# Optimization experiments

Hardware: AMD Instinct MI355X
Metric: run time of the kernel (lower is better)

Reference implementation:

```python
import jax, jax.numpy as jnp
import numpy as np

N_NODES = 100000
N_EDGES = 1600000
D_FEAT = 64


def setup_inputs() -> dict:
    key = jax.random.key(0)
    k1, k2, k3, k4, k5 = jax.random.split(key, 5)
    feat = jax.random.normal(k1, (N_NODES, D_FEAT), dtype=jnp.float32)
    weight = jax.random.normal(k2, (N_EDGES, 1), dtype=jnp.float32)
    bias = jax.random.normal(k3, (D_FEAT,), dtype=jnp.float32)
    src = jax.random.randint(k4, (N_EDGES,), 0, N_NODES, dtype=jnp.int32)
    dst = jax.random.randint(k5, (N_EDGES,), 0, N_NODES, dtype=jnp.int32)
    return {"feat": feat, "weight": weight, "bias": bias, "src": src, "dst": dst}


def reference(feat, weight, bias, src, dst):
    # Weighted SpMM: out[v] = sum_{e: dst[e]==v} weight[e] * feat[src[e]] + bias
    messages = feat[src] * weight  # [E, D] gather + per-edge scale
    out = jax.ops.segment_sum(messages, dst, num_segments=N_NODES)  # [N, D]
    return out + bias
```

## Files before the change

### kernel.cpp

```cpp
#include <hip/hip_runtime.h>

#define N_NODES 100000
#define N_EDGES 1600000
#define D_FEAT  64
#define NFEAT_ELEM (N_NODES * D_FEAT)

#define BUCK_SHIFT 6
#define BUCK_NODES 64
#define NBUCK ((N_NODES + BUCK_NODES - 1) / BUCK_NODES)
#define NB1 (NBUCK + 1)

#define CHUNK   8192
#define NCHUNK  ((N_EDGES + CHUNK - 1) / CHUNK)
#define BIN_BLK 512
#define BIN_EPT (CHUNK / BIN_BLK)
#define SCAN_PER ((NBUCK + BIN_BLK - 1) / BIN_BLK)
#define PREP_BLOCKS 128

#define GB_BLK   512
#define GB_NODES 128
#define NGRP ((NBUCK + 1) / 2)
#define GB_CAP   2816
#define GB_EPT   6

typedef float          vf4 __attribute__((ext_vector_type(4)));
typedef float          vf2 __attribute__((ext_vector_type(2)));
typedef int            vi2 __attribute__((ext_vector_type(2)));
typedef unsigned short vu4 __attribute__((ext_vector_type(4)));
typedef unsigned short ushort_t;

#define TBL_BYTES  (NCHUNK * NB1 * 2)
#define OFF_TBL    0
#define OFF_EP     (((OFF_TBL + TBL_BYTES) + 255) & ~255)
#define OFF_FEATB  (OFF_EP + N_EDGES * 8)
#define WS_MED     (size_t)OFF_FEATB
#define WS_FULL    (size_t)(OFF_FEATB + (size_t)NFEAT_ELEM * 2)

template <int BF16>
__global__ __launch_bounds__(BIN_BLK) void k_bin(const int* __restrict__ src,
                                                 const int* __restrict__ dst,
                                                 const float* __restrict__ weight,
                                                 const float* __restrict__ feat,
                                                 ushort_t* __restrict__ featb,
                                                 ushort_t* __restrict__ tbl,
                                                 vi2* __restrict__ ep) {
    if (blockIdx.x >= NCHUNK) {
        if (!BF16) return;
        const int stride = PREP_BLOCKS * BIN_BLK;
        for (int i = (blockIdx.x - NCHUNK) * BIN_BLK + threadIdx.x;
             i < NFEAT_ELEM / 4; i += stride) {
            vf4 x = ((const vf4*)feat)[i];
            vu4 r;
#pragma unroll
            for (int k = 0; k < 4; ++k) {
                unsigned bb = __float_as_uint(x[k]);
                r[k] = (ushort_t)((bb + 0x7fffu + ((bb >> 16) & 1u)) >> 16);
            }
            ((vu4*)featb)[i] = r;
        }
        return;
    }

    __shared__ vi2 schunk[CHUNK];
    __shared__ int lcnt[NBUCK];
    __shared__ int ss[BIN_BLK];
    const int t = threadIdx.x;
    const int c = blockIdx.x;
    const int e0 = c * CHUNK;
    const int chunkN = (N_EDGES - e0 < CHUNK) ? (N_EDGES - e0) : CHUNK;

    for (int i = t; i < NBUCK; i += BIN_BLK) lcnt[i] = 0;
    __syncthreads();

    int bk[BIN_EPT], rk[BIN_EPT], xk[BIN_EPT], wk[BIN_EPT];
#pragma unroll
    for (int k = 0; k < BIN_EPT; ++k) {
        const int e = e0 + t + k * BIN_BLK;
        bk[k] = -1;
        if (e < N_EDGES) {
            int v = __builtin_nontemporal_load(dst + e);
            int s = __builtin_nontemporal_load(src + e);
            wk[k] = __builtin_nontemporal_load((const int*)weight + e);
            bk[k] = v >> BUCK_SHIFT;
            xk[k] = ((v & (BUCK_NODES - 1)) << 24) | s;
            rk[k] = atomicAdd(&lcnt[bk[k]], 1);
        }
    }
    __syncthreads();

    int v7[SCAN_PER];
    const int lo = t * SCAN_PER;
    int s = 0;
#pragma unroll
    for (int k = 0; k < SCAN_PER; ++k) {
        const int i = lo + k;
        v7[k] = (i < NBUCK) ? lcnt[i] : 0;
        s += v7[k];
    }
    ss[t] = s;
    __syncthreads();
    for (int off = 1; off < BIN_BLK; off <<= 1) {
        int x = (t >= off) ? ss[t - off] : 0;
        __syncthreads();
        ss[t] += x;
        __syncthreads();
    }
    int run = ss[t] - s;
    ushort_t* row = tbl + (size_t)c * NB1;
#pragma unroll
    for (int k = 0; k < SCAN_PER; ++k) {
        const int i = lo + k;
        if (i < NBUCK) {
            row[i] = (ushort_t)run;
            lcnt[i] = run;
            run += v7[k];
        }
    }
    if (t == BIN_BLK - 1) row[NBUCK] = (ushort_t)chunkN;
    __syncthreads();

#pragma unroll
    for (int k = 0; k < BIN_EPT; ++k)
        if (bk[k] >= 0) schunk[lcnt[bk[k]] + rk[k]] = (vi2){xk[k], wk[k]};
    __syncthreads();

    for (int i = t; i < chunkN; i += BIN_BLK)
        ep[e0 + i] = schunk[i];
}

template <int BF16>
__global__ __launch_bounds__(GB_BLK, 8) void k_sgather(const float* __restrict__ feat,
                                                       const ushort_t* __restrict__ featb,
                                                       const float* __restrict__ bias,
                                                       const ushort_t* __restrict__ tbl,
                                                       const vi2* __restrict__ ep,
                                                       float* __restrict__ out) {
    __shared__ vi2      srt[GB_CAP];
    __shared__ int      basearr[GB_BLK];
    __shared__ ushort_t o0arr[GB_BLK];
    __shared__ ushort_t o1arr[GB_BLK];
    __shared__ int      cnt[GB_NODES], off[GB_NODES];
    __shared__ int      wsum[8];
    __shared__ int      wpre[9];
    __shared__ int      c64tot;

    const int t = threadIdx.x;
    const int lane = t & 63;
    const int wid = t >> 6;
    const int grp = blockIdx.x;
    const int b0 = grp * 2;
    if (t < GB_NODES) cnt[t] = 0;

    int o0 = 0, o1 = 0, o2 = 0;
    if (t < NCHUNK) {
        const ushort_t* rowp = tbl + (size_t)t * NB1 + b0;
        unsigned u = *(const unsigned*)rowp;
        o0 = (int)(u & 0xFFFFu);
        o1 = (int)(u >> 16);
        o2 = (b0 + 2 <= NBUCK) ? (int)rowp[2] : o1;
    }
    o0arr[t] = (ushort_t)o0;
    o1arr[t] = (ushort_t)o1;
    const int len = o2 - o0;

    int incl = len;
#pragma unroll
    for (int o = 1; o < 64; o <<= 1) {
        int x = __shfl_up(incl, o);
        if (lane >= o) incl += x;
    }
    if (lane == 63) wsum[wid] = incl;
    __syncthreads();
    if (t == 0) {
        int run = 0;
#pragma unroll
        for (int i2 = 0; i2 < 8; ++i2) { wpre[i2] = run; run += wsum[i2]; }
        wpre[8] = run;
    }
    __syncthreads();
    const int nTot = wpre[8];
    basearr[t] = wpre[wid] + incl - len;
    __syncthreads();

    const int nStg = nTot < GB_CAP ? nTot : GB_CAP;
    int   xk[GB_EPT];
    float wk[GB_EPT];
    int   rk[GB_EPT];
#pragma unroll
    for (int k = 0; k < GB_EPT; ++k) {
        const int p = t + k * GB_BLK;
        xk[k] = -1;
        if (p < nStg) {
            int c = 0;
#pragma unroll
            for (int s2 = 256; s2 > 0; s2 >>= 1) {
                int m = c + s2;
                if (m < GB_BLK && basearr[m] <= p) c = m;
            }
            const int e = (int)o0arr[c] + (p - basearr[c]);
            vi2 v = ep[(size_t)c * CHUNK + e];
            int r = ((e >= (int)o1arr[c]) ? 64 : 0) + (int)((unsigned)v.x >> 24);
            xk[k] = (v.x & 0xFFFFFF) | (r << 24);
            wk[k] = __int_as_float(v.y);
            rk[k] = atomicAdd(&cnt[r], 1);
        }
    }
    __syncthreads();

    {
        int v = (t < GB_NODES) ? cnt[t] : 0;
        int inc2 = v;
#pragma unroll
        for (int o = 1; o < 64; o <<= 1) {
            int x = __shfl_up(inc2, o);
            if (lane >= o) inc2 += x;
        }
        if (t == 63) c64tot = inc2;
        __syncthreads();
        if (t >= 64 && t < 128) inc2 += c64tot;
        if (t < GB_NODES) off[t] = inc2;
        __syncthreads();
    }

#pragma unroll
    for (int k = 0; k < GB_EPT; ++k) {
        if (xk[k] != -1) {
            int r = (unsigned)xk[k] >> 24;
            srt[off[r] - cnt[r] + rk[k]] = (vi2){xk[k], __float_as_int(wk[k])};
        }
    }
    __syncthreads();

    const int col = lane & 31;
    const int half = lane >> 5;
    const vf2 b2 = ((const vf2*)bias)[col];
    for (int rp = 0; rp < 8; ++rp) {
        const int rA = wid * 16 + rp;
        const int rB = rA + 8;
        const int ccA = cnt[rA], s0A = off[rA] - ccA;
        const int ccB = cnt[rB], s0B = off[rB] - ccB;
        float a0A = 0.f, a1A = 0.f, a0B = 0.f, a1B = 0.f;
        const int ccM = ccA > ccB ? ccA : ccB;
        for (int i = 0; i < ccM; i += 8) {
            float wA[4], wB[4];
            unsigned dA[4], dB[4];
            vf2 fA[4], fB[4];
#pragma unroll
            for (int k = 0; k < 4; ++k) {
                const int ei = i + 2 * k + half;
                vi2 e = (ei < ccA) ? srt[s0A + ei] : (vi2){0, 0};
                wA[k] = __int_as_float(e.y);
                const int sidx = e.x & 0xFFFFFF;
                if (BF16) dA[k] = *((const unsigned*)(featb + (size_t)sidx * D_FEAT) + col);
                else      fA[k] = *((const vf2*)(feat + (size_t)sidx * D_FEAT) + col);
            }
#pragma unroll
            for (int k = 0; k < 4; ++k) {
                const int ei = i + 2 * k + half;
                vi2 e = (ei < ccB) ? srt[s0B + ei] : (vi2){0, 0};
                wB[k] = __int_as_float(e.y);
                const int sidx = e.x & 0xFFFFFF;
                if (BF16) dB[k] = *((const unsigned*)(featb + (size_t)sidx * D_FEAT) + col);
                else      fB[k] = *((const vf2*)(feat + (size_t)sidx * D_FEAT) + col);
            }
            if (BF16) {
#pragma unroll
                for (int k = 0; k < 4; ++k) {
                    a0A = fmaf(wA[k], __uint_as_float(dA[k] << 16), a0A);
                    a1A = fmaf(wA[k], __uint_as_float(dA[k] & 0xFFFF0000u), a1A);
                    a0B = fmaf(wB[k], __uint_as_float(dB[k] << 16), a0B);
                    a1B = fmaf(wB[k], __uint_as_float(dB[k] & 0xFFFF0000u), a1B);
                }
            } else {
#pragma unroll
                for (int k = 0; k < 4; ++k) {
                    a0A = fmaf(wA[k], fA[k].x, a0A);
                    a1A = fmaf(wA[k], fA[k].y, a1A);
                    a0B = fmaf(wB[k], fB[k].x, a0B);
                    a1B = fmaf(wB[k], fB[k].y, a1B);
                }
            }
        }
        a0A += __shfl_xor(a0A, 32);
        a1A += __shfl_xor(a1A, 32);
        a0B += __shfl_xor(a0B, 32);
        a1B += __shfl_xor(a1B, 32);
        const int nodeA = grp * GB_NODES + rA;
        const int nodeB = grp * GB_NODES + rB;
        if (half == 0 && nodeA < N_NODES) {
            vf2 o = {a0A + b2.x, a1A + b2.y};
            __builtin_nontemporal_store(o, (vf2*)(out + (size_t)nodeA * D_FEAT) + col);
        }
        if (half == 0 && nodeB < N_NODES) {
            vf2 o = {a0B + b2.x, a1B + b2.y};
            __builtin_nontemporal_store(o, (vf2*)(out + (size_t)nodeB * D_FEAT) + col);
        }
    }
    __syncthreads();

    for (int p = GB_CAP + t; p < nTot; p += GB_BLK) {
        int c = 0;
#pragma unroll
        for (int s2 = 256; s2 > 0; s2 >>= 1) {
            int m = c + s2;
            if (m < GB_BLK && basearr[m] <= p) c = m;
        }
        const int e = (int)o0arr[c] + (p - basearr[c]);
        vi2 v = ep[(size_t)c * CHUNK + e];
        int r = ((e >= (int)o1arr[c]) ? 64 : 0) + (int)((unsigned)v.x >> 24);
        int node = grp * GB_NODES + r;
        float w = __int_as_float(v.y);
        int sidx = v.x & 0xFFFFFF;
        if (node < N_NODES)
            for (int d2 = 0; d2 < D_FEAT; ++d2)
                atomicAdd(&out[(size_t)node * D_FEAT + d2], w * feat[(size_t)sidx * D_FEAT + d2]);
    }
}

__global__ void init_out_kernel(const float* __restrict__ bias,
                                float* __restrict__ out) {
    int i = blockIdx.x * blockDim.x + threadIdx.x;
    if (i < N_NODES * D_FEAT) out[i] = bias[i & (D_FEAT - 1)];
}

__global__ void edge_scatter_kernel(const float* __restrict__ feat,
                                    const float* __restrict__ weight,
                                    const int* __restrict__ src,
                                    const int* __restrict__ dst,
                                    float* __restrict__ out) {
    int e = blockIdx.x * 4 + (threadIdx.x >> 6);
    int lane = threadIdx.x & 63;
    if (e < N_EDGES) {
        atomicAdd(&out[dst[e] * D_FEAT + lane], weight[e] * feat[src[e] * D_FEAT + lane]);
    }
}

extern "C" void kernel_launch(void* const* d_in, const int* in_sizes, int n_in,
                              void* d_out, int out_size, void* d_ws, size_t ws_size,
                              hipStream_t stream) {
    const float* feat   = (const float*)d_in[0];
    const float* weight = (const float*)d_in[1];
    const float* bias   = (const float*)d_in[2];
    const int*   src    = (const int*)d_in[3];
    const int*   dst    = (const int*)d_in[4];
    float* out = (float*)d_out;

    if (ws_size < WS_MED) {
        int total = N_NODES * D_FEAT;
        init_out_kernel<<<(total + 255) / 256, 256, 0, stream>>>(bias, out);
        edge_scatter_kernel<<<(N_EDGES + 3) / 4, 256, 0, stream>>>(feat, weight, src, dst, out);
        return;
    }

    char* ws = (char*)d_ws;
    ushort_t* tbl   = (ushort_t*)(ws + OFF_TBL);
    vi2*      ep    = (vi2*)(ws + OFF_EP);
    ushort_t* featb = (ushort_t*)(ws + OFF_FEATB);
    const bool use_bf16 = (ws_size >= WS_FULL);

    if (use_bf16) {
        k_bin<1><<<NCHUNK + PREP_BLOCKS, BIN_BLK, 0, stream>>>(src, dst, weight, feat, featb, tbl, ep);
        k_sgather<1><<<NGRP, GB_BLK, 0, stream>>>(feat, featb, bias, tbl, ep, out);
    } else {
        k_bin<0><<<NCHUNK, BIN_BLK, 0, stream>>>(src, dst, weight, feat, featb, tbl, ep);
        k_sgather<0><<<NGRP, GB_BLK, 0, stream>>>(feat, featb, bias, tbl, ep, out);
    }
}
```

Measured before the change: 64.08 us.

## Quantize gathered features to int8 with per-row scale folded into edge weight

Replaces the bf16 copy of the node features with an int8 copy that has one scale per row. The scale is multiplied into each edge weight during staging, so the gather loop reads 2 bytes per lane instead of 4 and converts int8 to float. This halves the random-gather traffic, at the cost of an extra scale lookup per edge and a large loss of precision that may break accuracy tolerance.

```diff
diff --git a/kernel.cpp b/kernel.cpp
--- a/kernel.cpp
+++ b/kernel.cpp
@@ -26,37 +26,46 @@
 typedef float          vf4 __attribute__((ext_vector_type(4)));
 typedef float          vf2 __attribute__((ext_vector_type(2)));
 typedef int            vi2 __attribute__((ext_vector_type(2)));
-typedef unsigned short vu4 __attribute__((ext_vector_type(4)));
 typedef unsigned short ushort_t;
+typedef signed char    s8_t;
 
 #define TBL_BYTES  (NCHUNK * NB1 * 2)
 #define OFF_TBL    0
 #define OFF_EP     (((OFF_TBL + TBL_BYTES) + 255) & ~255)
-#define OFF_FEATB  (OFF_EP + N_EDGES * 8)
-#define WS_MED     (size_t)OFF_FEATB
-#define WS_FULL    (size_t)(OFF_FEATB + (size_t)NFEAT_ELEM * 2)
-
-template <int BF16>
+#define OFF_SCALE  (OFF_EP + N_EDGES * 8)
+#define OFF_FEATQ  (OFF_SCALE + N_NODES * 4)
+#define WS_MED     (size_t)OFF_SCALE
+#define WS_FULL    (size_t)(OFF_FEATQ + (size_t)NFEAT_ELEM)
+
+template <int QNT>
 __global__ __launch_bounds__(BIN_BLK) void k_bin(const int* __restrict__ src,
                                                  const int* __restrict__ dst,
                                                  const float* __restrict__ weight,
                                                  const float* __restrict__ feat,
-                                                 ushort_t* __restrict__ featb,
+                                                 s8_t* __restrict__ featq,
+                                                 float* __restrict__ fscale,
                                                  ushort_t* __restrict__ tbl,
                                                  vi2* __restrict__ ep) {
+    const int t = threadIdx.x;
     if (blockIdx.x >= NCHUNK) {
-        if (!BF16) return;
-        const int stride = PREP_BLOCKS * BIN_BLK;
-        for (int i = (blockIdx.x - NCHUNK) * BIN_BLK + threadIdx.x;
-             i < NFEAT_ELEM / 4; i += stride) {
-            vf4 x = ((const vf4*)feat)[i];
-            vu4 r;
-#pragma unroll
-            for (int k = 0; k < 4; ++k) {
-                unsigned bb = __float_as_uint(x[k]);
-                r[k] = (ushort_t)((bb + 0x7fffu + ((bb >> 16) & 1u)) >> 16);
-            }
-            ((vu4*)featb)[i] = r;
+        if (!QNT) return;
+        const int lane = t & 63;
+        const int wid = t >> 6;
+        const int wgid = (blockIdx.x - NCHUNK) * (BIN_BLK / 64) + wid;
+        const int nw = PREP_BLOCKS * (BIN_BLK / 64);
+        const int hl = lane & 31;
+        for (int pr = wgid; pr < N_NODES / 2; pr += nw) {
+            const int row = pr * 2 + (lane >> 5);
+            const vf2 x = *((const vf2*)(feat + (size_t)row * D_FEAT) + hl);
+            float m = fmaxf(fabsf(x.x), fabsf(x.y));
+#pragma unroll
+            for (int o = 16; o; o >>= 1) m = fmaxf(m, __shfl_xor(m, o));
+            const float rs = m > 0.f ? 127.0f / m : 0.f;
+            const int qa = __float2int_rn(x.x * rs);
+            const int qb = __float2int_rn(x.y * rs);
+            *((ushort_t*)(featq + (size_t)row * D_FEAT) + hl) =
+                (ushort_t)((qa & 0xFF) | ((qb & 0xFF) << 8));
+            if (hl == 0) fscale[row] = m * (1.0f / 127.0f);
         }
         return;
     }
@@ -64,7 +73,6 @@
     __shared__ vi2 schunk[CHUNK];
     __shared__ int lcnt[NBUCK];
     __shared__ int ss[BIN_BLK];
-    const int t = threadIdx.x;
     const int c = blockIdx.x;
     const int e0 = c * CHUNK;
     const int chunkN = (N_EDGES - e0 < CHUNK) ? (N_EDGES - e0) : CHUNK;
@@ -128,9 +136,10 @@
         ep[e0 + i] = schunk[i];
 }
 
-template <int BF16>
+template <int QNT>
 __global__ __launch_bounds__(GB_BLK, 8) void k_sgather(const float* __restrict__ feat,
-                                                       const ushort_t* __restrict__ featb,
+                                                       const s8_t* __restrict__ featq,
+                                                       const float* __restrict__ fscale,
                                                        const float* __restrict__ bias,
                                                        const ushort_t* __restrict__ tbl,
                                                        const vi2* __restrict__ ep,
@@ -200,8 +209,11 @@
             const int e = (int)o0arr[c] + (p - basearr[c]);
             vi2 v = ep[(size_t)c * CHUNK + e];
             int r = ((e >= (int)o1arr[c]) ? 64 : 0) + (int)((unsigned)v.x >> 24);
-            xk[k] = (v.x & 0xFFFFFF) | (r << 24);
-            wk[k] = __int_as_float(v.y);
+            const int sidx = v.x & 0xFFFFFF;
+            xk[k] = sidx | (r << 24);
+            float w = __int_as_float(v.y);
+            if (QNT) w *= fscale[sidx];
+            wk[k] = w;
             rk[k] = atomicAdd(&cnt[r], 1);
         }
     }
@@ -243,7 +255,7 @@
         const int ccM = ccA > ccB ? ccA : ccB;
         for (int i = 0; i < ccM; i += 8) {
             float wA[4], wB[4];
-            unsigned dA[4], dB[4];
+            unsigned qA[4], qB[4];
             vf2 fA[4], fB[4];
 #pragma unroll
             for (int k = 0; k < 4; ++k) {
@@ -251,8 +263,8 @@
                 vi2 e = (ei < ccA) ? srt[s0A + ei] : (vi2){0, 0};
                 wA[k] = __int_as_float(e.y);
                 const int sidx = e.x & 0xFFFFFF;
-                if (BF16) dA[k] = *((const unsigned*)(featb + (size_t)sidx * D_FEAT) + col);
-                else      fA[k] = *((const vf2*)(feat + (size_t)sidx * D_FEAT) + col);
+                if (QNT) qA[k] = *((const ushort_t*)(featq + (size_t)sidx * D_FEAT) + col);
+                else     fA[k] = *((const vf2*)(feat + (size_t)sidx * D_FEAT) + col);
             }
 #pragma unroll
             for (int k = 0; k < 4; ++k) {
@@ -260,16 +272,16 @@
                 vi2 e = (ei < ccB) ? srt[s0B + ei] : (vi2){0, 0};
                 wB[k] = __int_as_float(e.y);
                 const int sidx = e.x & 0xFFFFFF;
-                if (BF16) dB[k] = *((const unsigned*)(featb + (size_t)sidx * D_FEAT) + col);
-                else      fB[k] = *((const vf2*)(feat + (size_t)sidx * D_FEAT) + col);
+                if (QNT) qB[k] = *((const ushort_t*)(featq + (size_t)sidx * D_FEAT) + col);
+                else     fB[k] = *((const vf2*)(feat + (size_t)sidx * D_FEAT) + col);
             }
-            if (BF16) {
+            if (QNT) {
 #pragma unroll
                 for (int k = 0; k < 4; ++k) {
-                    a0A = fmaf(wA[k], __uint_as_float(dA[k] << 16), a0A);
-                    a1A = fmaf(wA[k], __uint_as_float(dA[k] & 0xFFFF0000u), a1A);
-                    a0B = fmaf(wB[k], __uint_as_float(dB[k] << 16), a0B);
-                    a1B = fmaf(wB[k], __uint_as_float(dB[k] & 0xFFFF0000u), a1B);
+                    a0A = fmaf(wA[k], (float)(int)(s8_t)(qA[k] & 0xFF), a0A);
+                    a1A = fmaf(wA[k], (float)(int)(s8_t)(qA[k] >> 8), a1A);
+                    a0B = fmaf(wB[k], (float)(int)(s8_t)(qB[k] & 0xFF), a0B);
+                    a1B = fmaf(wB[k], (float)(int)(s8_t)(qB[k] >> 8), a1B);
                 }
             } else {
 #pragma unroll
@@ -353,16 +365,17 @@
     }
 
     char* ws = (char*)d_ws;
-    ushort_t* tbl   = (ushort_t*)(ws + OFF_TBL);
-    vi2*      ep    = (vi2*)(ws + OFF_EP);
-    ushort_t* featb = (ushort_t*)(ws + OFF_FEATB);
-    const bool use_bf16 = (ws_size >= WS_FULL);
-
-    if (use_bf16) {
-        k_bin<1><<<NCHUNK + PREP_BLOCKS, BIN_BLK, 0, stream>>>(src, dst, weight, feat, featb, tbl, ep);
-        k_sgather<1><<<NGRP, GB_BLK, 0, stream>>>(feat, featb, bias, tbl, ep, out);
+    ushort_t* tbl    = (ushort_t*)(ws + OFF_TBL);
+    vi2*      ep     = (vi2*)(ws + OFF_EP);
+    float*    fscale = (float*)(ws + OFF_SCALE);
+    s8_t*     featq  = (s8_t*)(ws + OFF_FEATQ);
+    const bool use_q = (ws_size >= WS_FULL);
+
+    if (use_q) {
+        k_bin<1><<<NCHUNK + PREP_BLOCKS, BIN_BLK, 0, stream>>>(src, dst, weight, feat, featq, fscale, tbl, ep);
+        k_sgather<1><<<NGRP, GB_BLK, 0, stream>>>(feat, featq, fscale, bias, tbl, ep, out);
     } else {
-        k_bin<0><<<NCHUNK, BIN_BLK, 0, stream>>>(src, dst, weight, feat, featb, tbl, ep);
-        k_sgather<0><<<NGRP, GB_BLK, 0, stream>>>(feat, featb, bias, tbl, ep, out);
-    }
-}
+        k_bin<0><<<NCHUNK, BIN_BLK, 0, stream>>>(src, dst, weight, feat, featq, fscale, tbl, ep);
+        k_sgather<0><<<NGRP, GB_BLK, 0, stream>>>(feat, featq, fscale, bias, tbl, ep, out);
+    }
+}
```

Result: slower. 87.69 us (+36.8%).
